# Performance work log

Measured on AMD Instinct MI355X. Metric: run time of the kernel, lower is better.

Reference implementation:

```python
import jax, jax.numpy as jnp
import numpy as np

DIM = 384
HEADS = 6
EPS = 1e-5
SCALE = DIM ** -0.5  # note: original uses full dim, not head_dim


def _dwconv_bn(x, w, stride, g, b, m, v):
    # x: [B, C, H, W], w: [C, 1, 3, 3] depthwise
    y = jax.lax.conv_general_dilated(
        x, w, window_strides=(stride, stride), padding=((1, 1), (1, 1)),
        dimension_numbers=('NCHW', 'OIHW', 'NCHW'), feature_group_count=DIM)
    # BatchNorm2d inference form
    inv = jax.lax.rsqrt(v + EPS)
    y = (y - m[None, :, None, None]) * (inv * g)[None, :, None, None] + b[None, :, None, None]
    # b c h w -> b (h w) c
    B, C, H, W = y.shape
    return y.reshape(B, C, H * W).transpose(0, 2, 1)


def setup_inputs() -> dict:
    key = jax.random.key(0)
    ks = jax.random.split(key, 24)
    d = {}
    d['x'] = jax.random.normal(ks[0], (8, 3136, DIM), jnp.float32)
    d['h'] = 56
    d['w'] = 56
    i = 1
    for nm in ('q', 'k', 'v'):
        d[f'conv_{nm}'] = jax.random.normal(ks[i], (DIM, 1, 3, 3), jnp.float32) * 0.1; i += 1
        d[f'bn{nm}_s'] = jnp.ones((DIM,), jnp.float32)
        d[f'bn{nm}_b'] = jnp.zeros((DIM,), jnp.float32)
        d[f'bn{nm}_m'] = jax.random.normal(ks[i], (DIM,), jnp.float32) * 0.1; i += 1
        d[f'bn{nm}_v'] = jax.random.uniform(ks[i], (DIM,), jnp.float32) + 0.5; i += 1
    s = DIM ** -0.5
    d['wq'] = jax.random.normal(ks[i], (DIM, DIM), jnp.float32) * s; i += 1
    d['wk'] = jax.random.normal(ks[i], (DIM, DIM), jnp.float32) * s; i += 1
    d['wv'] = jax.random.normal(ks[i], (DIM, DIM), jnp.float32) * s; i += 1
    d['w_last'] = jax.random.normal(ks[i], (DIM, DIM), jnp.float32) * s; i += 1
    d['b_last'] = jnp.zeros((DIM,), jnp.float32)
    return d


def reference(x, h, w, conv_q, bnq_s, bnq_b, bnq_m, bnq_v,
              conv_k, bnk_s, bnk_b, bnk_m, bnk_v,
              conv_v, bnv_s, bnv_b, bnv_m, bnv_v,
              wq, wk, wv, w_last, b_last):
    B, T, C = x.shape
    xim = x.transpose(0, 2, 1).reshape(B, C, h, w)  # b (h w) c -> b c h w
    q = _dwconv_bn(xim, conv_q, 1, bnq_s, bnq_b, bnq_m, bnq_v)  # [B, h*w, C]
    k = _dwconv_bn(xim, conv_k, 2, bnk_s, bnk_b, bnk_m, bnk_v)  # [B, hw/4, C]
    v = _dwconv_bn(xim, conv_v, 2, bnv_s, bnv_b, bnv_m, bnv_v)
    # linear projections (torch Linear: y = x @ W.T), split heads
    def heads(t, W):
        y = jnp.einsum('btc,oc->bto', t, W)
        Bt, Tt, _ = y.shape
        return y.reshape(Bt, Tt, HEADS, C // HEADS).transpose(0, 2, 1, 3)
    qh, kh, vh = heads(q, wq), heads(k, wk), heads(v, wv)
    attn = jax.nn.softmax(jnp.einsum('bhld,bhtd->bhlt', qh, kh) * SCALE, axis=-1)
    o = jnp.einsum('bhlt,bhtd->bhld', attn, vh)  # [B, H, L, d]
    o = o.transpose(0, 2, 1, 3).reshape(B, T, C)
    return jnp.einsum('btc,oc->bto', o, w_last) + b_last
```

## Files before the change

kernel.cpp:

```cpp
#include <hip/hip_runtime.h>
#include <hip/hip_bf16.h>

typedef __bf16 bf16;
typedef __attribute__((ext_vector_type(8))) __bf16 bf16x8;
typedef __attribute__((ext_vector_type(4))) __bf16 bf16x4;
typedef __attribute__((ext_vector_type(4))) float floatx4;

#define MFMA16(a, b, c) __builtin_amdgcn_mfma_f32_16x16x32_bf16((a), (b), (c), 0, 0, 0)

#define DIM 384
#define T1 3136
#define T2 784
#define T2P 832
#define B_ 8
#define EPSV 1e-5f

__device__ __forceinline__ void gload_lds16(const bf16* g, bf16* l) {
  __builtin_amdgcn_global_load_lds(
      (const __attribute__((address_space(1))) void*)g,
      (__attribute__((address_space(3))) void*)l, 16, 0, 0);
}

__global__ void conv_fused_kernel(const float* __restrict__ x,
    const float* __restrict__ wqc, const float* __restrict__ gq, const float* __restrict__ bq,
    const float* __restrict__ mq, const float* __restrict__ vq,
    const float* __restrict__ wkc, const float* __restrict__ gk, const float* __restrict__ bk,
    const float* __restrict__ mk, const float* __restrict__ vk,
    const float* __restrict__ wvc, const float* __restrict__ gv, const float* __restrict__ bv,
    const float* __restrict__ mv, const float* __restrict__ vvv,
    bf16* __restrict__ qout, bf16* __restrict__ kout, bf16* __restrict__ vout,
    const float* __restrict__ w0, const float* __restrict__ w1,
    const float* __restrict__ w2, const float* __restrict__ w3,
    bf16* __restrict__ d0, bf16* __restrict__ d1,
    bf16* __restrict__ d2, bf16* __restrict__ d3) {
  int blk = blockIdx.x;
  int c = threadIdx.x;
  int gid = blk * DIM + c;
  if (gid < 147456) {
    d0[gid] = (bf16)w0[gid]; d1[gid] = (bf16)w1[gid];
    d2[gid] = (bf16)w2[gid]; d3[gid] = (bf16)w3[gid];
  }
  int xg = blk % 14;
  int y = (blk / 14) % 56;
  int b = blk / (14 * 56);
  int x0 = xg * 4;
  const float* xb = x + (size_t)b * T1 * DIM;
  float in[3][6];
#pragma unroll
  for (int r = 0; r < 3; ++r) {
    int yy = y + r - 1;
#pragma unroll
    for (int cc = 0; cc < 6; ++cc) {
      int xc = x0 + cc - 1;
      in[r][cc] = (yy >= 0 && yy < 56 && xc >= 0 && xc < 56)
                      ? xb[(yy * 56 + xc) * DIM + c] : 0.f;
    }
  }
  {
    float wr[9];
#pragma unroll
    for (int i = 0; i < 9; ++i) wr[i] = wqc[c * 9 + i];
    float a = rsqrtf(vq[c] + EPSV) * gq[c];
    float bia = bq[c] - mq[c] * a;
#pragma unroll
    for (int p = 0; p < 4; ++p) {
      float s = 0.f;
#pragma unroll
      for (int r = 0; r < 3; ++r)
#pragma unroll
        for (int dx = 0; dx < 3; ++dx) s += in[r][p + dx] * wr[r * 3 + dx];
      qout[((size_t)b * T1 + y * 56 + x0 + p) * DIM + c] = (bf16)(s * a + bia);
    }
  }
  if ((y & 1) == 0) {
    int y2 = y >> 1;
    float wk9[9], wv9[9];
#pragma unroll
    for (int i = 0; i < 9; ++i) { wk9[i] = wkc[c * 9 + i]; wv9[i] = wvc[c * 9 + i]; }
    float ak = rsqrtf(vk[c] + EPSV) * gk[c];
    float av = rsqrtf(vvv[c] + EPSV) * gv[c];
    float bik = bk[c] - mk[c] * ak;
    float biv = bv[c] - mv[c] * av;
#pragma unroll
    for (int p2 = 0; p2 < 2; ++p2) {
      float sk = 0.f, sv = 0.f;
#pragma unroll
      for (int r = 0; r < 3; ++r)
#pragma unroll
        for (int dx = 0; dx < 3; ++dx) {
          float xv = in[r][2 * p2 + dx];
          sk += xv * wk9[r * 3 + dx];
          sv += xv * wv9[r * 3 + dx];
        }
      size_t o = ((size_t)b * T2 + y2 * 28 + (x0 >> 1) + p2) * DIM + c;
      kout[o] = (bf16)(sk * ak + bik);
      vout[o] = (bf16)(sv * av + biv);
    }
  }
}

#define BK 32
#define BUFSZ (128 * BK)
__device__ __forceinline__
void gemm_body(const bf16* A, const bf16* Bw, void* out, const float* bias,
               int mode, float scale, int m0, int n0, bf16* Al, bf16* Bl) {
  int tid = threadIdx.x;
  int w = tid >> 6, lane = tid & 63;
  int wm = w >> 1, wn = w & 1;
  int l16 = lane & 15, quad = lane >> 4;
  floatx4 acc[4][4];
#pragma unroll
  for (int i = 0; i < 4; ++i)
#pragma unroll
    for (int j = 0; j < 4; ++j) acc[i][j] = (floatx4){0.f, 0.f, 0.f, 0.f};

  int srow = w * 32 + (lane >> 2);
  int scol = (lane & 3) * 8;
  const bf16* ag0 = &A[(size_t)(m0 + srow) * DIM + scol];
  const bf16* ag1 = ag0 + (size_t)16 * DIM;
  const bf16* bg0 = &Bw[(size_t)(n0 + srow) * DIM + scol];
  const bf16* bg1 = bg0 + (size_t)16 * DIM;
  int lofs0 = (w * 32) * BK;
  int lofs1 = (w * 32 + 16) * BK;

  gload_lds16(ag0, Al + lofs0);
  gload_lds16(ag1, Al + lofs1);
  gload_lds16(bg0, Bl + lofs0);
  gload_lds16(bg1, Bl + lofs1);

  const int NS = DIM / BK;
#pragma unroll
  for (int s = 0; s < NS; ++s) {
    const int cb = s & 1;
    if (s + 1 < NS) {
      const int k = (s + 1) * BK;
      bf16* an = Al + (cb ^ 1) * BUFSZ;
      bf16* bn = Bl + (cb ^ 1) * BUFSZ;
      gload_lds16(ag0 + k, an + lofs0);
      gload_lds16(ag1 + k, an + lofs1);
      gload_lds16(bg0 + k, bn + lofs0);
      gload_lds16(bg1 + k, bn + lofs1);
      asm volatile("s_waitcnt vmcnt(4)" ::: "memory");
    } else {
      asm volatile("s_waitcnt vmcnt(0)" ::: "memory");
    }
    __builtin_amdgcn_s_barrier();
    const bf16* Ac = Al + cb * BUFSZ;
    const bf16* Bc = Bl + cb * BUFSZ;
    bf16x8 af[4], bfr[4];
#pragma unroll
    for (int i = 0; i < 4; ++i) {
      af[i]  = *(const bf16x8*)&Ac[(wm * 64 + i * 16 + l16) * BK + quad * 8];
      bfr[i] = *(const bf16x8*)&Bc[(wn * 64 + i * 16 + l16) * BK + quad * 8];
    }
#pragma unroll
    for (int i = 0; i < 4; ++i)
#pragma unroll
      for (int j = 0; j < 4; ++j)
        acc[i][j] = MFMA16(af[i], bfr[j], acc[i][j]);
    asm volatile("s_waitcnt lgkmcnt(0)" ::: "memory");
    __builtin_amdgcn_s_barrier();
  }
#pragma unroll
  for (int i = 0; i < 4; ++i) {
#pragma unroll
    for (int j = 0; j < 4; ++j) {
#pragma unroll
      for (int rr = 0; rr < 4; ++rr) {
        int row = m0 + wm * 64 + i * 16 + quad * 4 + rr;
        int col = n0 + wn * 64 + j * 16 + l16;
        float v = acc[i][j][rr];
        if (mode == 3) {
          ((float*)out)[(size_t)row * DIM + col] = v + bias[col];
        } else if (mode == 2) {
          int b = row / T2;
          int t = row - b * T2;
          ((bf16*)out)[((size_t)b * DIM + col) * T2P + t] = (bf16)v;
        } else {
          ((bf16*)out)[(size_t)row * DIM + col] = (bf16)(v * scale);
        }
      }
    }
  }
}

__global__ __launch_bounds__(256)
void qkv_gemm_kernel(const bf16* q_act, const bf16* k_act, const bf16* v_act,
                     const bf16* wqb, const bf16* wkb, const bf16* wvb,
                     bf16* Qp, bf16* Kp, bf16* Vtp, float qscale) {
  __shared__ bf16 Al[2 * BUFSZ];
  __shared__ bf16 Bl[2 * BUFSZ];
  int bx = blockIdx.x;
  int xp = bx & 7, j = bx >> 3;
  int t = (j / 3) * 24 + xp * 3 + (j % 3);
  if (t >= 882) return;
  const bf16 *A, *Bw; void* out; int mode, ti; float scale;
  if (t < 588)      { A = q_act; Bw = wqb; out = Qp;  mode = 1; scale = qscale; ti = t; }
  else if (t < 735) { A = k_act; Bw = wkb; out = Kp;  mode = 0; scale = 1.f; ti = t - 588; }
  else              { A = v_act; Bw = wvb; out = Vtp; mode = 2; scale = 1.f; ti = t - 735; }
  gemm_body(A, Bw, out, nullptr, mode, scale, (ti / 3) * 128, (ti % 3) * 128, Al, Bl);
}

__global__ __launch_bounds__(256)
void last_gemm_kernel(const bf16* A, const bf16* Bw, float* out, const float* bias) {
  __shared__ bf16 Al[2 * BUFSZ];
  __shared__ bf16 Bl[2 * BUFSZ];
  int bx = blockIdx.x;
  int xp = bx & 7, j = bx >> 3;
  int t = (j / 3) * 24 + xp * 3 + (j % 3);
  if (t >= 588) return;
  gemm_body(A, Bw, out, bias, 3, 1.f, (t / 3) * 128, (t % 3) * 128, Al, Bl);
}

__global__ __launch_bounds__(256, 4)
void attn_kernel(const bf16* __restrict__ Qp, const bf16* __restrict__ Kp,
                 const bf16* __restrict__ Vt, bf16* __restrict__ Ob) {
  __shared__ bf16 Kl[64 * 64];
  __shared__ bf16 Vl[64 * 64];
  __shared__ bf16 Pl[4][2][16 * 64];
  int bx = blockIdx.x;
  int xcd = bx & 7, j = bx >> 3;
  int g = xcd + 8 * (j / 25);
  int qblk = j % 25;
  int h = g % 6;
  int b = g / 6;
  int tid = threadIdx.x, w = tid >> 6, lane = tid & 63;
  int l16 = lane & 15, quad = lane >> 4;
  int q0w = qblk * 128 + w * 32;

  bf16x8 qf[2][2];
#pragma unroll
  for (int qt = 0; qt < 2; ++qt) {
    int qi = q0w + qt * 16 + l16;
    qi = qi < T1 ? qi : T1 - 1;
    const bf16* qp = &Qp[((size_t)b * T1 + qi) * DIM + h * 64];
    qf[qt][0] = *(const bf16x8*)&qp[quad * 8];
    qf[qt][1] = *(const bf16x8*)&qp[32 + quad * 8];
  }
  floatx4 oacc[2][4];
#pragma unroll
  for (int qt = 0; qt < 2; ++qt)
#pragma unroll
    for (int dt = 0; dt < 4; ++dt) oacc[qt][dt] = (floatx4){0.f, 0.f, 0.f, 0.f};
  float lsum[2] = {0.f, 0.f};

  int rsub = lane >> 3;
  int chnk = (lane & 7) ^ rsub;
  const bf16* kg0 = &Kp[((size_t)b * T2 + w * 16 + rsub) * DIM + h * 64 + chnk * 8];
  const bf16* kg1 = kg0 + (size_t)8 * DIM;
  const bf16* vg0 = &Vt[((size_t)b * DIM + h * 64 + w * 16 + rsub) * T2P + chnk * 8];
  const bf16* vg1 = vg0 + (size_t)8 * T2P;
  bf16* kl0 = &Kl[(w * 16) * 64];
  bf16* kl1 = &Kl[(w * 16 + 8) * 64];
  bf16* vl0 = &Vl[(w * 16) * 64];
  bf16* vl1 = &Vl[(w * 16 + 8) * 64];

  int key = l16 & 7;

  for (int it = 0; it < 12; ++it) {
    __syncthreads();
    gload_lds16(kg0, kl0);
    gload_lds16(kg1, kl1);
    gload_lds16(vg0, vl0);
    gload_lds16(vg1, vl1);
    __syncthreads();
#pragma unroll
    for (int mt = 0; mt < 4; ++mt) {
      int krow = (mt * 16 + l16) * 64;
      bf16x8 kf0 = *(const bf16x8*)&Kl[krow + ((quad) ^ key) * 8];
      bf16x8 kf1 = *(const bf16x8*)&Kl[krow + ((quad + 4) ^ key) * 8];
      int pchunk = (((mt * 2 + (quad >> 1)) ^ key) << 3) + (quad & 1) * 4;
#pragma unroll
      for (int qt = 0; qt < 2; ++qt) {
        floatx4 z = (floatx4){0.f, 0.f, 0.f, 0.f};
        z = MFMA16(kf0, qf[qt][0], z);
        z = MFMA16(kf1, qf[qt][1], z);
        float p0 = __builtin_amdgcn_exp2f(z[0]);
        float p1 = __builtin_amdgcn_exp2f(z[1]);
        float p2 = __builtin_amdgcn_exp2f(z[2]);
        float p3 = __builtin_amdgcn_exp2f(z[3]);
        lsum[qt] += (p0 + p1) + (p2 + p3);
        bf16x4 pw = (bf16x4){(bf16)p0, (bf16)p1, (bf16)p2, (bf16)p3};
        *(bf16x4*)&Pl[w][qt][l16 * 64 + pchunk] = pw;
      }
    }
#pragma unroll
    for (int kt = 0; kt < 2; ++kt) {
      int rchunk = ((kt * 4 + quad) ^ key) << 3;
      bf16x8 pf0 = *(const bf16x8*)&Pl[w][0][l16 * 64 + rchunk];
      bf16x8 pf1 = *(const bf16x8*)&Pl[w][1][l16 * 64 + rchunk];
#pragma unroll
      for (int dt = 0; dt < 4; ++dt) {
        bf16x8 vf = *(const bf16x8*)&Vl[(dt * 16 + l16) * 64 + ((kt * 4 + quad) ^ key) * 8];
        oacc[0][dt] = MFMA16(vf, pf0, oacc[0][dt]);
        oacc[1][dt] = MFMA16(vf, pf1, oacc[1][dt]);
      }
    }
    kg0 += (size_t)64 * DIM; kg1 += (size_t)64 * DIM;
    vg0 += 64; vg1 += 64;
  }
  {
    const bf16* kptr = &Kp[((size_t)b * T2 + 768 + l16) * DIM + h * 64 + quad * 8];
    const bf16* vptr = &Vt[((size_t)b * DIM + h * 64 + l16) * T2P + 768 + quad * 8];
    bf16x8 kf0 = *(const bf16x8*)(kptr);
    bf16x8 kf1 = *(const bf16x8*)(kptr + 32);
    bf16x4 zz = (bf16x4){(bf16)0.f, (bf16)0.f, (bf16)0.f, (bf16)0.f};
    int pc0 = ((((quad >> 1)) ^ key) << 3) + (quad & 1) * 4;
    int pc1 = (((2 + (quad >> 1)) ^ key) << 3) + (quad & 1) * 4;
#pragma unroll
    for (int qt = 0; qt < 2; ++qt) {
      floatx4 z = (floatx4){0.f, 0.f, 0.f, 0.f};
      z = MFMA16(kf0, qf[qt][0], z);
      z = MFMA16(kf1, qf[qt][1], z);
      float p0 = __builtin_amdgcn_exp2f(z[0]);
      float p1 = __builtin_amdgcn_exp2f(z[1]);
      float p2 = __builtin_amdgcn_exp2f(z[2]);
      float p3 = __builtin_amdgcn_exp2f(z[3]);
      lsum[qt] += (p0 + p1) + (p2 + p3);
      bf16x4 pw = (bf16x4){(bf16)p0, (bf16)p1, (bf16)p2, (bf16)p3};
      *(bf16x4*)&Pl[w][qt][l16 * 64 + pc0] = pw;
      *(bf16x4*)&Pl[w][qt][l16 * 64 + pc1] = zz;
    }
    int rchunk = (quad ^ key) << 3;
    bf16x8 pf0 = *(const bf16x8*)&Pl[w][0][l16 * 64 + rchunk];
    bf16x8 pf1 = *(const bf16x8*)&Pl[w][1][l16 * 64 + rchunk];
#pragma unroll
    for (int dt = 0; dt < 4; ++dt) {
      bf16x8 vf = *(const bf16x8*)(vptr + (size_t)(dt * 16) * T2P);
      oacc[0][dt] = MFMA16(vf, pf0, oacc[0][dt]);
      oacc[1][dt] = MFMA16(vf, pf1, oacc[1][dt]);
    }
  }
#pragma unroll
  for (int qt = 0; qt < 2; ++qt) {
    float l = lsum[qt];
    l += __shfl_xor(l, 16);
    l += __shfl_xor(l, 32);
    float inv = 1.f / l;
    int qg = q0w + qt * 16 + l16;
    if (qg < T1) {
      bf16* op = &Ob[((size_t)b * T1 + qg) * DIM + h * 64];
#pragma unroll
      for (int dt = 0; dt < 4; ++dt) {
        floatx4 o = oacc[qt][dt];
        bf16x4 ov = (bf16x4){(bf16)(o[0] * inv), (bf16)(o[1] * inv),
                             (bf16)(o[2] * inv), (bf16)(o[3] * inv)};
        *(bf16x4*)&op[dt * 16 + quad * 4] = ov;
      }
    }
  }
}

extern "C" void kernel_launch(void* const* d_in, const int* in_sizes, int n_in,
                              void* d_out, int out_size, void* d_ws, size_t ws_size,
                              hipStream_t stream) {
  (void)in_sizes; (void)n_in; (void)out_size; (void)ws_size;
  const float* x      = (const float*)d_in[0];
  const float* conv_q = (const float*)d_in[3];
  const float* bnq_s  = (const float*)d_in[4];
  const float* bnq_b  = (const float*)d_in[5];
  const float* bnq_m  = (const float*)d_in[6];
  const float* bnq_v  = (const float*)d_in[7];
  const float* conv_k = (const float*)d_in[8];
  const float* bnk_s  = (const float*)d_in[9];
  const float* bnk_b  = (const float*)d_in[10];
  const float* bnk_m  = (const float*)d_in[11];
  const float* bnk_v  = (const float*)d_in[12];
  const float* conv_v = (const float*)d_in[13];
  const float* bnv_s  = (const float*)d_in[14];
  const float* bnv_b  = (const float*)d_in[15];
  const float* bnv_m  = (const float*)d_in[16];
  const float* bnv_v  = (const float*)d_in[17];
  const float* wq     = (const float*)d_in[18];
  const float* wk     = (const float*)d_in[19];
  const float* wv     = (const float*)d_in[20];
  const float* wl     = (const float*)d_in[21];
  const float* b_last = (const float*)d_in[22];

  char* ws = (char*)d_ws;
  bf16* q_act = (bf16*)(ws + 0);
  bf16* k_act = (bf16*)(ws + 19267584);
  bf16* v_act = (bf16*)(ws + 24084480);
  bf16* Qp    = (bf16*)(ws + 28901376);
  bf16* Kp    = (bf16*)(ws + 48168960);
  bf16* Vtp   = (bf16*)(ws + 52985856);
  bf16* wqb   = (bf16*)(ws + 58097664);
  bf16* wkb   = wqb + 147456;
  bf16* wvb   = wkb + 147456;
  bf16* wlb   = wvb + 147456;

  const float QSCALE = 0.05103103630798288f * 1.4426950408889634f;

  conv_fused_kernel<<<B_ * 56 * 14, DIM, 0, stream>>>(
      x,
      conv_q, bnq_s, bnq_b, bnq_m, bnq_v,
      conv_k, bnk_s, bnk_b, bnk_m, bnk_v,
      conv_v, bnv_s, bnv_b, bnv_m, bnv_v,
      q_act, k_act, v_act,
      wq, wk, wv, wl, wqb, wkb, wvb, wlb);

  qkv_gemm_kernel<<<888, 256, 0, stream>>>(q_act, k_act, v_act, wqb, wkb, wvb,
                                           Qp, Kp, Vtp, QSCALE);

  attn_kernel<<<25 * 6 * B_, 256, 0, stream>>>(Qp, Kp, Vtp, q_act);

  last_gemm_kernel<<<600, 256, 0, stream>>>(q_act, wlb, (float*)d_out, b_last);
}
```

Measured before the change: 248.3 us.

## Double-buffer K/V LDS tiles in attention to overlap loads with compute

The attention kernel now keeps two LDS buffers for the K and V tiles. It prefetches the next 64-key tile with global_load_lds while the current tile is being computed, and uses explicit vmcnt waits and barriers in place of the two __syncthreads per iteration. This is meant to hide global load latency behind the MFMA and exp work. In exchange it doubles K/V LDS usage and lowers the occupancy hint from 4 to 3 blocks per CU, which can cut latency hiding across blocks.

```diff
diff --git a/kernel.cpp b/kernel.cpp
--- a/kernel.cpp
+++ b/kernel.cpp
@@ -212,11 +212,11 @@
   gemm_body(A, Bw, out, bias, 3, 1.f, (t / 3) * 128, (t % 3) * 128, Al, Bl);
 }
 
-__global__ __launch_bounds__(256, 4)
+__global__ __launch_bounds__(256, 3)
 void attn_kernel(const bf16* __restrict__ Qp, const bf16* __restrict__ Kp,
                  const bf16* __restrict__ Vt, bf16* __restrict__ Ob) {
-  __shared__ bf16 Kl[64 * 64];
-  __shared__ bf16 Vl[64 * 64];
+  __shared__ bf16 Kl[2][64 * 64];
+  __shared__ bf16 Vl[2][64 * 64];
   __shared__ bf16 Pl[4][2][16 * 64];
   int bx = blockIdx.x;
   int xcd = bx & 7, j = bx >> 3;
@@ -250,25 +250,39 @@
   const bf16* kg1 = kg0 + (size_t)8 * DIM;
   const bf16* vg0 = &Vt[((size_t)b * DIM + h * 64 + w * 16 + rsub) * T2P + chnk * 8];
   const bf16* vg1 = vg0 + (size_t)8 * T2P;
-  bf16* kl0 = &Kl[(w * 16) * 64];
-  bf16* kl1 = &Kl[(w * 16 + 8) * 64];
-  bf16* vl0 = &Vl[(w * 16) * 64];
-  bf16* vl1 = &Vl[(w * 16 + 8) * 64];
+  int lo0 = (w * 16) * 64;
+  int lo1 = (w * 16 + 8) * 64;
 
   int key = l16 & 7;
 
+  gload_lds16(kg0, &Kl[0][lo0]);
+  gload_lds16(kg1, &Kl[0][lo1]);
+  gload_lds16(vg0, &Vl[0][lo0]);
+  gload_lds16(vg1, &Vl[0][lo1]);
+  kg0 += (size_t)64 * DIM; kg1 += (size_t)64 * DIM;
+  vg0 += 64; vg1 += 64;
+
   for (int it = 0; it < 12; ++it) {
-    __syncthreads();
-    gload_lds16(kg0, kl0);
-    gload_lds16(kg1, kl1);
-    gload_lds16(vg0, vl0);
-    gload_lds16(vg1, vl1);
-    __syncthreads();
+    const int cb = it & 1;
+    if (it < 11) {
+      gload_lds16(kg0, &Kl[cb ^ 1][lo0]);
+      gload_lds16(kg1, &Kl[cb ^ 1][lo1]);
+      gload_lds16(vg0, &Vl[cb ^ 1][lo0]);
+      gload_lds16(vg1, &Vl[cb ^ 1][lo1]);
+      kg0 += (size_t)64 * DIM; kg1 += (size_t)64 * DIM;
+      vg0 += 64; vg1 += 64;
+      asm volatile("s_waitcnt vmcnt(4)" ::: "memory");
+    } else {
+      asm volatile("s_waitcnt vmcnt(0)" ::: "memory");
+    }
+    __builtin_amdgcn_s_barrier();
+    const bf16* Kc = Kl[cb];
+    const bf16* Vc = Vl[cb];
 #pragma unroll
     for (int mt = 0; mt < 4; ++mt) {
       int krow = (mt * 16 + l16) * 64;
-      bf16x8 kf0 = *(const bf16x8*)&Kl[krow + ((quad) ^ key) * 8];
-      bf16x8 kf1 = *(const bf16x8*)&Kl[krow + ((quad + 4) ^ key) * 8];
+      bf16x8 kf0 = *(const bf16x8*)&Kc[krow + ((quad) ^ key) * 8];
+      bf16x8 kf1 = *(const bf16x8*)&Kc[krow + ((quad + 4) ^ key) * 8];
       int pchunk = (((mt * 2 + (quad >> 1)) ^ key) << 3) + (quad & 1) * 4;
 #pragma unroll
       for (int qt = 0; qt < 2; ++qt) {
@@ -291,13 +305,13 @@
       bf16x8 pf1 = *(const bf16x8*)&Pl[w][1][l16 * 64 + rchunk];
 #pragma unroll
       for (int dt = 0; dt < 4; ++dt) {
-        bf16x8 vf = *(const bf16x8*)&Vl[(dt * 16 + l16) * 64 + ((kt * 4 + quad) ^ key) * 8];
+        bf16x8 vf = *(const bf16x8*)&Vc[(dt * 16 + l16) * 64 + ((kt * 4 + quad) ^ key) * 8];
         oacc[0][dt] = MFMA16(vf, pf0, oacc[0][dt]);
         oacc[1][dt] = MFMA16(vf, pf1, oacc[1][dt]);
       }
     }
-    kg0 += (size_t)64 * DIM; kg1 += (size_t)64 * DIM;
-    vg0 += 64; vg1 += 64;
+    asm volatile("s_waitcnt lgkmcnt(0)" ::: "memory");
+    __builtin_amdgcn_s_barrier();
   }
   {
     const bf16* kptr = &Kp[((size_t)b * T2 + 768 + l16) * DIM + h * 64 + quad * 8];
```

Result: no change. 250.0 us (+0.7%).

## Switch attention to 32x32 MFMA and keep P in registers via lane shuffles

Applied to the files above, without the earlier changes.

The attention kernel moves from 16x16x32 to 32x32x16 bf16 MFMA tiles, with each wave covering 32 queries in one tile. The softmax probabilities are packed to bf16 and exchanged between half-waves with shuffles, so they go straight into the PV MFMA as operands. This removes the per-wave LDS round trip for P and its shared memory. The cost is larger accumulator register use, which may lower occupancy, plus extra shuffle and select instructions.

```diff
diff --git a/kernel.cpp b/kernel.cpp
--- a/kernel.cpp
+++ b/kernel.cpp
@@ -4,9 +4,13 @@
 typedef __bf16 bf16;
 typedef __attribute__((ext_vector_type(8))) __bf16 bf16x8;
 typedef __attribute__((ext_vector_type(4))) __bf16 bf16x4;
+typedef __attribute__((ext_vector_type(2))) __bf16 bf16x2;
 typedef __attribute__((ext_vector_type(4))) float floatx4;
+typedef __attribute__((ext_vector_type(16))) float floatx16;
+typedef unsigned int u32;
 
 #define MFMA16(a, b, c) __builtin_amdgcn_mfma_f32_16x16x32_bf16((a), (b), (c), 0, 0, 0)
+#define MFMA32(a, b, c) __builtin_amdgcn_mfma_f32_32x32x16_bf16((a), (b), (c), 0, 0, 0)
 
 #define DIM 384
 #define T1 3136
@@ -19,6 +23,11 @@
   __builtin_amdgcn_global_load_lds(
       (const __attribute__((address_space(1))) void*)g,
       (__attribute__((address_space(3))) void*)l, 16, 0, 0);
+}
+
+__device__ __forceinline__ u32 pk2(float a, float b) {
+  bf16x2 t = (bf16x2){(bf16)a, (bf16)b};
+  return *reinterpret_cast<u32*>(&t);
 }
 
 __global__ void conv_fused_kernel(const float* __restrict__ x,
@@ -217,7 +226,6 @@
                  const bf16* __restrict__ Vt, bf16* __restrict__ Ob) {
   __shared__ bf16 Kl[64 * 64];
   __shared__ bf16 Vl[64 * 64];
-  __shared__ bf16 Pl[4][2][16 * 64];
   int bx = blockIdx.x;
   int xcd = bx & 7, j = bx >> 3;
   int g = xcd + 8 * (j / 25);
@@ -225,24 +233,21 @@
   int h = g % 6;
   int b = g / 6;
   int tid = threadIdx.x, w = tid >> 6, lane = tid & 63;
-  int l16 = lane & 15, quad = lane >> 4;
+  int l32 = lane & 31, hi = lane >> 5;
   int q0w = qblk * 128 + w * 32;
 
-  bf16x8 qf[2][2];
-#pragma unroll
-  for (int qt = 0; qt < 2; ++qt) {
-    int qi = q0w + qt * 16 + l16;
+  bf16x8 qf[4];
+  {
+    int qi = q0w + l32;
     qi = qi < T1 ? qi : T1 - 1;
     const bf16* qp = &Qp[((size_t)b * T1 + qi) * DIM + h * 64];
-    qf[qt][0] = *(const bf16x8*)&qp[quad * 8];
-    qf[qt][1] = *(const bf16x8*)&qp[32 + quad * 8];
-  }
-  floatx4 oacc[2][4];
-#pragma unroll
-  for (int qt = 0; qt < 2; ++qt)
-#pragma unroll
-    for (int dt = 0; dt < 4; ++dt) oacc[qt][dt] = (floatx4){0.f, 0.f, 0.f, 0.f};
-  float lsum[2] = {0.f, 0.f};
+#pragma unroll
+    for (int kk = 0; kk < 4; ++kk) qf[kk] = *(const bf16x8*)&qp[kk * 16 + hi * 8];
+  }
+  floatx16 oacc[2];
+  oacc[0] = (floatx16)0.f;
+  oacc[1] = (floatx16)0.f;
+  float lsum = 0.f;
 
   int rsub = lane >> 3;
   int chnk = (lane & 7) ^ rsub;
@@ -255,7 +260,7 @@
   bf16* vl0 = &Vl[(w * 16) * 64];
   bf16* vl1 = &Vl[(w * 16 + 8) * 64];
 
-  int key = l16 & 7;
+  int key = lane & 7;
 
   for (int it = 0; it < 12; ++it) {
     __syncthreads();
@@ -265,87 +270,96 @@
     gload_lds16(vg1, vl1);
     __syncthreads();
 #pragma unroll
-    for (int mt = 0; mt < 4; ++mt) {
-      int krow = (mt * 16 + l16) * 64;
-      bf16x8 kf0 = *(const bf16x8*)&Kl[krow + ((quad) ^ key) * 8];
-      bf16x8 kf1 = *(const bf16x8*)&Kl[krow + ((quad + 4) ^ key) * 8];
-      int pchunk = (((mt * 2 + (quad >> 1)) ^ key) << 3) + (quad & 1) * 4;
-#pragma unroll
-      for (int qt = 0; qt < 2; ++qt) {
-        floatx4 z = (floatx4){0.f, 0.f, 0.f, 0.f};
-        z = MFMA16(kf0, qf[qt][0], z);
-        z = MFMA16(kf1, qf[qt][1], z);
-        float p0 = __builtin_amdgcn_exp2f(z[0]);
-        float p1 = __builtin_amdgcn_exp2f(z[1]);
-        float p2 = __builtin_amdgcn_exp2f(z[2]);
-        float p3 = __builtin_amdgcn_exp2f(z[3]);
-        lsum[qt] += (p0 + p1) + (p2 + p3);
-        bf16x4 pw = (bf16x4){(bf16)p0, (bf16)p1, (bf16)p2, (bf16)p3};
-        *(bf16x4*)&Pl[w][qt][l16 * 64 + pchunk] = pw;
+    for (int tt = 0; tt < 2; ++tt) {
+      floatx16 s = (floatx16)0.f;
+#pragma unroll
+      for (int kk = 0; kk < 4; ++kk) {
+        bf16x8 kf = *(const bf16x8*)&Kl[(tt * 32 + l32) * 64 + ((kk * 2 + hi) ^ key) * 8];
+        s = MFMA32(kf, qf[kk], s);
       }
-    }
-#pragma unroll
-    for (int kt = 0; kt < 2; ++kt) {
-      int rchunk = ((kt * 4 + quad) ^ key) << 3;
-      bf16x8 pf0 = *(const bf16x8*)&Pl[w][0][l16 * 64 + rchunk];
-      bf16x8 pf1 = *(const bf16x8*)&Pl[w][1][l16 * 64 + rchunk];
-#pragma unroll
-      for (int dt = 0; dt < 4; ++dt) {
-        bf16x8 vf = *(const bf16x8*)&Vl[(dt * 16 + l16) * 64 + ((kt * 4 + quad) ^ key) * 8];
-        oacc[0][dt] = MFMA16(vf, pf0, oacc[0][dt]);
-        oacc[1][dt] = MFMA16(vf, pf1, oacc[1][dt]);
+      float e[16];
+#pragma unroll
+      for (int r = 0; r < 16; ++r) {
+        e[r] = __builtin_amdgcn_exp2f(s[r]);
+        lsum += e[r];
+      }
+#pragma unroll
+      for (int kkl = 0; kkl < 2; ++kkl) {
+        int r0 = kkl * 8;
+        u32 pA = pk2(e[r0 + 0], e[r0 + 1]);
+        u32 pB = pk2(e[r0 + 2], e[r0 + 3]);
+        u32 pC = pk2(e[r0 + 4], e[r0 + 5]);
+        u32 pD = pk2(e[r0 + 6], e[r0 + 7]);
+        u32 sA = __shfl_xor(pA, 32);
+        u32 sB = __shfl_xor(pB, 32);
+        u32 sC = __shfl_xor(pC, 32);
+        u32 sD = __shfl_xor(pD, 32);
+        union { u32 u[4]; bf16x8 v; } pf;
+        pf.u[0] = hi ? sC : pA;
+        pf.u[1] = hi ? sD : pB;
+        pf.u[2] = hi ? pC : sA;
+        pf.u[3] = hi ? pD : sB;
+        int kk = tt * 2 + kkl;
+#pragma unroll
+        for (int dt = 0; dt < 2; ++dt) {
+          bf16x8 vf = *(const bf16x8*)&Vl[(dt * 32 + l32) * 64 + ((kk * 2 + hi) ^ key) * 8];
+          oacc[dt] = MFMA32(vf, pf.v, oacc[dt]);
+        }
       }
     }
     kg0 += (size_t)64 * DIM; kg1 += (size_t)64 * DIM;
     vg0 += 64; vg1 += 64;
   }
   {
-    const bf16* kptr = &Kp[((size_t)b * T2 + 768 + l16) * DIM + h * 64 + quad * 8];
-    const bf16* vptr = &Vt[((size_t)b * DIM + h * 64 + l16) * T2P + 768 + quad * 8];
-    bf16x8 kf0 = *(const bf16x8*)(kptr);
-    bf16x8 kf1 = *(const bf16x8*)(kptr + 32);
-    bf16x4 zz = (bf16x4){(bf16)0.f, (bf16)0.f, (bf16)0.f, (bf16)0.f};
-    int pc0 = ((((quad >> 1)) ^ key) << 3) + (quad & 1) * 4;
-    int pc1 = (((2 + (quad >> 1)) ^ key) << 3) + (quad & 1) * 4;
-#pragma unroll
-    for (int qt = 0; qt < 2; ++qt) {
-      floatx4 z = (floatx4){0.f, 0.f, 0.f, 0.f};
-      z = MFMA16(kf0, qf[qt][0], z);
-      z = MFMA16(kf1, qf[qt][1], z);
-      float p0 = __builtin_amdgcn_exp2f(z[0]);
-      float p1 = __builtin_amdgcn_exp2f(z[1]);
-      float p2 = __builtin_amdgcn_exp2f(z[2]);
-      float p3 = __builtin_amdgcn_exp2f(z[3]);
-      lsum[qt] += (p0 + p1) + (p2 + p3);
-      bf16x4 pw = (bf16x4){(bf16)p0, (bf16)p1, (bf16)p2, (bf16)p3};
-      *(bf16x4*)&Pl[w][qt][l16 * 64 + pc0] = pw;
-      *(bf16x4*)&Pl[w][qt][l16 * 64 + pc1] = zz;
-    }
-    int rchunk = (quad ^ key) << 3;
-    bf16x8 pf0 = *(const bf16x8*)&Pl[w][0][l16 * 64 + rchunk];
-    bf16x8 pf1 = *(const bf16x8*)&Pl[w][1][l16 * 64 + rchunk];
-#pragma unroll
-    for (int dt = 0; dt < 4; ++dt) {
-      bf16x8 vf = *(const bf16x8*)(vptr + (size_t)(dt * 16) * T2P);
-      oacc[0][dt] = MFMA16(vf, pf0, oacc[0][dt]);
-      oacc[1][dt] = MFMA16(vf, pf1, oacc[1][dt]);
-    }
-  }
-#pragma unroll
-  for (int qt = 0; qt < 2; ++qt) {
-    float l = lsum[qt];
-    l += __shfl_xor(l, 16);
-    l += __shfl_xor(l, 32);
-    float inv = 1.f / l;
-    int qg = q0w + qt * 16 + l16;
-    if (qg < T1) {
-      bf16* op = &Ob[((size_t)b * T1 + qg) * DIM + h * 64];
-#pragma unroll
-      for (int dt = 0; dt < 4; ++dt) {
-        floatx4 o = oacc[qt][dt];
-        bf16x4 ov = (bf16x4){(bf16)(o[0] * inv), (bf16)(o[1] * inv),
-                             (bf16)(o[2] * inv), (bf16)(o[3] * inv)};
-        *(bf16x4*)&op[dt * 16 + quad * 4] = ov;
+    int tq = 768 + l32;
+    tq = tq < T2 ? tq : T2 - 1;
+    const bf16* kp2 = &Kp[((size_t)b * T2 + tq) * DIM + h * 64];
+    floatx16 s = (floatx16)0.f;
+#pragma unroll
+    for (int kk = 0; kk < 4; ++kk) {
+      bf16x8 kf = *(const bf16x8*)&kp2[kk * 16 + hi * 8];
+      s = MFMA32(kf, qf[kk], s);
+    }
+    float e[8];
+#pragma unroll
+    for (int r = 0; r < 8; ++r) {
+      e[r] = __builtin_amdgcn_exp2f(s[r]);
+      lsum += e[r];
+    }
+    u32 pA = pk2(e[0], e[1]);
+    u32 pB = pk2(e[2], e[3]);
+    u32 pC = pk2(e[4], e[5]);
+    u32 pD = pk2(e[6], e[7]);
+    u32 sA = __shfl_xor(pA, 32);
+    u32 sB = __shfl_xor(pB, 32);
+    u32 sC = __shfl_xor(pC, 32);
+    u32 sD = __shfl_xor(pD, 32);
+    union { u32 u[4]; bf16x8 v; } pf;
+    pf.u[0] = hi ? sC : pA;
+    pf.u[1] = hi ? sD : pB;
+    pf.u[2] = hi ? pC : sA;
+    pf.u[3] = hi ? pD : sB;
+#pragma unroll
+    for (int dt = 0; dt < 2; ++dt) {
+      const bf16* vp2 = &Vt[((size_t)b * DIM + h * 64 + dt * 32 + l32) * T2P + 768 + hi * 8];
+      bf16x8 vf = *(const bf16x8*)vp2;
+      oacc[dt] = MFMA32(vf, pf.v, oacc[dt]);
+    }
+  }
+  lsum += __shfl_xor(lsum, 32);
+  float inv = 1.f / lsum;
+  int qg = q0w + l32;
+  if (qg < T1) {
+    bf16* op = &Ob[((size_t)b * T1 + qg) * DIM + h * 64];
+#pragma unroll
+    for (int dt = 0; dt < 2; ++dt) {
+#pragma unroll
+      for (int gr = 0; gr < 4; ++gr) {
+        bf16x4 ov = (bf16x4){(bf16)(oacc[dt][gr * 4 + 0] * inv),
+                             (bf16)(oacc[dt][gr * 4 + 1] * inv),
+                             (bf16)(oacc[dt][gr * 4 + 2] * inv),
+                             (bf16)(oacc[dt][gr * 4 + 3] * inv)};
+        *(bf16x4*)&op[dt * 32 + gr * 8 + hi * 4] = ov;
       }
     }
   }
```

After: 247.8 us. About the same (-0.2%).
